# Performance work log

Hardware: AMD Instinct MI355X
Metric: run time of the kernel (lower is better)

## Reference

```python
import jax, jax.numpy as jnp
import numpy as np

EPSILON_BASE = 0.1
N_ITERS = 10


def setup_inputs() -> dict:
    key = jax.random.key(0)
    k1, k2 = jax.random.split(key)
    N, D = 8192, 512
    embeddings = jax.random.normal(k1, (N, D), dtype=jnp.float32)
    target_noise = jax.random.normal(k2, (N, D), dtype=jnp.float32)
    return {"embeddings": embeddings, "target_noise": target_noise}


def _l2_normalize(x, axis=1, eps=1e-12):
    # matches torch.nn.functional.normalize (divide by max(norm, eps))
    norm = jnp.sqrt(jnp.sum(x * x, axis=axis, keepdims=True))
    return x / jnp.maximum(norm, eps)


def _sinkhorn(x, y):
    n, d = x.shape
    # normalize_embeddings=True path
    x = _l2_normalize(x, axis=1)
    y = _l2_normalize(y, axis=1)
    epsilon = EPSILON_BASE * 2.0
    # squared euclidean cost: C[i,j] = ||x_i - y_j||^2  (cdist p=2, squared)
    sq_x = jnp.sum(x * x, axis=1, keepdims=True)          # (n,1)
    sq_y = jnp.sum(y * y, axis=1, keepdims=True)          # (n,1)
    C = jnp.maximum(sq_x + sq_y.T - 2.0 * (x @ y.T), 0.0)  # (n,n)
    log_K = -C / epsilon

    def body(carry, _):
        log_u, log_v = carry
        log_u = -jax.nn.logsumexp(log_K + log_v[None, :], axis=1)
        log_v = -jax.nn.logsumexp(log_K.T + log_u[None, :], axis=1)
        return (log_u, log_v), None

    init = (jnp.zeros(n, dtype=x.dtype), jnp.zeros(n, dtype=y.dtype))
    (log_u, log_v), _ = jax.lax.scan(body, init, None, length=N_ITERS)

    log_P = log_u[:, None] + log_K + log_v[None, :]
    P = jnp.clip(jnp.exp(log_P), 0.0, 1.0)
    distance = jnp.sum(P * C) / n

    # nan/inf fallback: 1 - mean cosine similarity (x, y already unit norm)
    fallback = 1.0 - jnp.mean(jnp.sum(x * y, axis=1))
    bad = jnp.isnan(distance) | jnp.isinf(distance)
    return jnp.where(bad, fallback, distance)


def reference(embeddings, target_noise):
    if embeddings.ndim == 3:
        embeddings = embeddings.reshape(-1, embeddings.shape[-1])
        target_noise = target_noise.reshape(-1, target_noise.shape[-1])
    return _sinkhorn(embeddings, target_noise)
```

## Files before the change

### kernel.cpp

```cpp
#include <hip/hip_runtime.h>
#include <hip/hip_bf16.h>
#include <stdint.h>

#define NROW 8192
#define DIM  512
#define LN2   0.6931471805599453f
#define TEN_LOG2E 14.426950408889634f

typedef __attribute__((ext_vector_type(8))) short short8;
typedef __attribute__((ext_vector_type(4))) float f32x4;
typedef __attribute__((ext_vector_type(2))) float f32x2;

__global__ __launch_bounds__(256) void init_kernel(float* __restrict__ v,
                                                   float* __restrict__ diagacc,
                                                   float* __restrict__ distacc) {
  const int g = blockIdx.x * 256 + threadIdx.x;
  v[g] = 1.0f;
  if (g == 0) { diagacc[0] = 0.f; distacc[0] = 0.f; }
}

__global__ __launch_bounds__(256) void normalize_kernel(
    const float* __restrict__ X, const float* __restrict__ Y,
    __hip_bfloat16* __restrict__ Xn, __hip_bfloat16* __restrict__ Yn,
    float* __restrict__ diagacc) {
  const int wave = threadIdx.x >> 6, lane = threadIdx.x & 63;
  float dsum = 0.f;
  #pragma unroll
  for (int rr = 0; rr < 4; rr++) {
    const int row = blockIdx.x * 16 + wave * 4 + rr;
    const float4* xr = (const float4*)(X + (size_t)row * DIM);
    const float4* yr = (const float4*)(Y + (size_t)row * DIM);
    float4 x0 = xr[lane], x1 = xr[lane + 64];
    float4 y0 = yr[lane], y1 = yr[lane + 64];
    float sx = x0.x*x0.x + x0.y*x0.y + x0.z*x0.z + x0.w*x0.w
             + x1.x*x1.x + x1.y*x1.y + x1.z*x1.z + x1.w*x1.w;
    float sy = y0.x*y0.x + y0.y*y0.y + y0.z*y0.z + y0.w*y0.w
             + y1.x*y1.x + y1.y*y1.y + y1.z*y1.z + y1.w*y1.w;
    float sxy = x0.x*y0.x + x0.y*y0.y + x0.z*y0.z + x0.w*y0.w
              + x1.x*y1.x + x1.y*y1.y + x1.z*y1.z + x1.w*y1.w;
    #pragma unroll
    for (int off = 1; off < 64; off <<= 1) {
      sx  += __shfl_xor(sx, off, 64);
      sy  += __shfl_xor(sy, off, 64);
      sxy += __shfl_xor(sxy, off, 64);
    }
    const float rx = 1.0f / fmaxf(sqrtf(sx), 1e-12f);
    const float ry = 1.0f / fmaxf(sqrtf(sy), 1e-12f);
    if (lane == 0) dsum += sxy * rx * ry;
    ushort4 px, py;
    { __hip_bfloat16 b;
      b = __float2bfloat16(x0.x*rx); px.x = *(unsigned short*)&b;
      b = __float2bfloat16(x0.y*rx); px.y = *(unsigned short*)&b;
      b = __float2bfloat16(x0.z*rx); px.z = *(unsigned short*)&b;
      b = __float2bfloat16(x0.w*rx); px.w = *(unsigned short*)&b;
      b = __float2bfloat16(y0.x*ry); py.x = *(unsigned short*)&b;
      b = __float2bfloat16(y0.y*ry); py.y = *(unsigned short*)&b;
      b = __float2bfloat16(y0.z*ry); py.z = *(unsigned short*)&b;
      b = __float2bfloat16(y0.w*ry); py.w = *(unsigned short*)&b;
    }
    ((ushort4*)(Xn + (size_t)row * DIM))[lane] = px;
    ((ushort4*)(Yn + (size_t)row * DIM))[lane] = py;
    { __hip_bfloat16 b;
      b = __float2bfloat16(x1.x*rx); px.x = *(unsigned short*)&b;
      b = __float2bfloat16(x1.y*rx); px.y = *(unsigned short*)&b;
      b = __float2bfloat16(x1.z*rx); px.z = *(unsigned short*)&b;
      b = __float2bfloat16(x1.w*rx); px.w = *(unsigned short*)&b;
      b = __float2bfloat16(y1.x*ry); py.x = *(unsigned short*)&b;
      b = __float2bfloat16(y1.y*ry); py.y = *(unsigned short*)&b;
      b = __float2bfloat16(y1.z*ry); py.z = *(unsigned short*)&b;
      b = __float2bfloat16(y1.w*ry); py.w = *(unsigned short*)&b;
    }
    ((ushort4*)(Xn + (size_t)row * DIM))[lane + 64] = px;
    ((ushort4*)(Yn + (size_t)row * DIM))[lane + 64] = py;
  }
  if (lane == 0) atomicAdd(diagacc, dsum);
}

__global__ __launch_bounds__(256) void gemm_kernel(
    const __hip_bfloat16* __restrict__ A, const __hip_bfloat16* __restrict__ B,
    uint8_t* __restrict__ K) {
  __shared__ __align__(16) char smem[20480];
  short* As = (short*)smem;
  short* Bs = (short*)(smem + 10240);
  int* tileT = (int*)smem;

  const int m0 = blockIdx.y * 128;
  const int n0 = blockIdx.x * 128;
  const int t = threadIdx.x;
  const int wave = t >> 6, lane = t & 63;
  const int wm = (wave & 1) * 64, wn = (wave >> 1) * 64;
  const int fr = lane & 15;
  const int fq = lane >> 4;

  f32x4 acc[4][4];
  #pragma unroll
  for (int i = 0; i < 4; i++)
    #pragma unroll
    for (int j = 0; j < 4; j++) acc[i][j] = (f32x4)0.f;

  const int L0 = t, L1 = t + 256;
  const int ar0 = L0 >> 2, ac0 = L0 & 3;
  const int ar1 = L1 >> 2, ac1 = L1 & 3;
  const int4* Ag = (const int4*)A;
  const int4* Bg = (const int4*)B;

  for (int kt = 0; kt < 16; ++kt) {
    const int kb = kt * 4;
    int4 a0 = Ag[(size_t)(m0 + ar0) * 64 + kb + ac0];
    int4 a1 = Ag[(size_t)(m0 + ar1) * 64 + kb + ac1];
    int4 b0 = Bg[(size_t)(n0 + ar0) * 64 + kb + ac0];
    int4 b1 = Bg[(size_t)(n0 + ar1) * 64 + kb + ac1];
    __syncthreads();
    ((int4*)As)[ar0 * 5 + ac0] = a0;
    ((int4*)As)[ar1 * 5 + ac1] = a1;
    ((int4*)Bs)[ar0 * 5 + ac0] = b0;
    ((int4*)Bs)[ar1 * 5 + ac1] = b1;
    __syncthreads();
    short8 af[4], bfr[4];
    #pragma unroll
    for (int i = 0; i < 4; i++) {
      af[i]  = *(const short8*)&As[(wm + i * 16 + fr) * 40 + fq * 8];
      bfr[i] = *(const short8*)&Bs[(wn + i * 16 + fr) * 40 + fq * 8];
    }
    #pragma unroll
    for (int i = 0; i < 4; i++)
      #pragma unroll
      for (int j = 0; j < 4; j++)
        acc[i][j] = __builtin_amdgcn_mfma_f32_16x16x32_bf16(af[i], bfr[j], acc[i][j], 0, 0, 0);
  }
  __syncthreads();
  #pragma unroll
  for (int i = 0; i < 4; i++) {
    #pragma unroll
    for (int j = 0; j < 4; j++) {
      const int Rq = (wm >> 2) + i * 4 + fq;
      const int Cc = wn + j * 16 + fr;
      float v0 = exp2f(fminf(acc[i][j][0], 1.0f) * TEN_LOG2E);
      float v1 = exp2f(fminf(acc[i][j][1], 1.0f) * TEN_LOG2E);
      float v2 = exp2f(fminf(acc[i][j][2], 1.0f) * TEN_LOG2E);
      float v3 = exp2f(fminf(acc[i][j][3], 1.0f) * TEN_LOG2E);
      int pk = 0;
      pk = __builtin_amdgcn_cvt_pk_fp8_f32(v0, v1, pk, false);
      pk = __builtin_amdgcn_cvt_pk_fp8_f32(v2, v3, pk, true);
      tileT[Cc * 33 + Rq] = pk;
    }
  }
  __syncthreads();
  const int rl = t >> 1;
  const int half = t & 1;
  const int rq = rl >> 2;
  const int rb = (rl & 3) * 8;
  uint8_t* Krow = K + (size_t)(m0 + rl) * NROW + n0 + half * 64;
  #pragma unroll
  for (int q = 0; q < 4; q++) {
    int out[4];
    #pragma unroll
    for (int d = 0; d < 4; d++) {
      const int c0 = (half * 16 + q * 4 + d) * 4;
      const unsigned w0 = (unsigned)tileT[(c0 + 0) * 33 + rq];
      const unsigned w1 = (unsigned)tileT[(c0 + 1) * 33 + rq];
      const unsigned w2 = (unsigned)tileT[(c0 + 2) * 33 + rq];
      const unsigned w3 = (unsigned)tileT[(c0 + 3) * 33 + rq];
      out[d] = (int)(((w0 >> rb) & 0xffu) | (((w1 >> rb) & 0xffu) << 8)
                   | (((w2 >> rb) & 0xffu) << 16) | (((w3 >> rb) & 0xffu) << 24));
    }
    int4 o; o.x = out[0]; o.y = out[1]; o.z = out[2]; o.w = out[3];
    ((int4*)Krow)[q] = o;
  }
}

__global__ __launch_bounds__(512) void fused_pass_kernel(
    const uint8_t* __restrict__ K, const float* __restrict__ v,
    float* __restrict__ u, float* __restrict__ partials) {
  __shared__ float wsum[8][8];
  __shared__ float ubc[8];
  const int t = threadIdx.x;
  const int wave = t >> 6, lane = t & 63;
  const int i0 = blockIdx.x * 32;

  float wv[16];
  {
    const float4* vp = (const float4*)(v + t * 16);
    ((float4*)wv)[0] = vp[0]; ((float4*)wv)[1] = vp[1];
    ((float4*)wv)[2] = vp[2]; ((float4*)wv)[3] = vp[3];
  }
  float acc[16];
  #pragma unroll
  for (int c = 0; c < 16; c++) acc[c] = 0.f;

  for (int b = 0; b < 4; b++) {
    const int rbase = i0 + b * 8;
    int4 kd[8];
    #pragma unroll
    for (int r = 0; r < 8; r++)
      kd[r] = *(const int4*)(K + (size_t)(rbase + r) * NROW + t * 16);
    float dot[8];
    #pragma unroll
    for (int r = 0; r < 8; r++) {
      const int* kp = (const int*)&kd[r];
      float d0 = 0.f, d1 = 0.f;
      #pragma unroll
      for (int q = 0; q < 4; q++) {
        f32x2 lo = __builtin_amdgcn_cvt_pk_f32_fp8(kp[q], false);
        f32x2 hi = __builtin_amdgcn_cvt_pk_f32_fp8(kp[q], true);
        d0 += lo.x * wv[4 * q] + lo.y * wv[4 * q + 1];
        d1 += hi.x * wv[4 * q + 2] + hi.y * wv[4 * q + 3];
      }
      dot[r] = d0 + d1;
    }
    #pragma unroll
    for (int r = 0; r < 8; r++)
      #pragma unroll
      for (int off = 1; off < 64; off <<= 1)
        dot[r] += __shfl_xor(dot[r], off, 64);
    if (lane == 0) {
      #pragma unroll
      for (int r = 0; r < 8; r++) wsum[wave][r] = dot[r];
    }
    __syncthreads();
    if (t < 8) {
      float s = wsum[0][t] + wsum[1][t] + wsum[2][t] + wsum[3][t]
              + wsum[4][t] + wsum[5][t] + wsum[6][t] + wsum[7][t];
      float uu = 1.0f / s;
      ubc[t] = uu;
      u[rbase + t] = uu;
    }
    __syncthreads();
    float ur[8];
    #pragma unroll
    for (int r = 0; r < 8; r++) ur[r] = ubc[r];
    #pragma unroll
    for (int r = 0; r < 8; r++) {
      const int* kp = (const int*)&kd[r];
      #pragma unroll
      for (int q = 0; q < 4; q++) {
        f32x2 lo = __builtin_amdgcn_cvt_pk_f32_fp8(kp[q], false);
        f32x2 hi = __builtin_amdgcn_cvt_pk_f32_fp8(kp[q], true);
        acc[4 * q]     += lo.x * ur[r];
        acc[4 * q + 1] += lo.y * ur[r];
        acc[4 * q + 2] += hi.x * ur[r];
        acc[4 * q + 3] += hi.y * ur[r];
      }
    }
  }
  float4* pp = (float4*)(partials + (size_t)blockIdx.x * NROW + t * 16);
  pp[0] = ((float4*)acc)[0]; pp[1] = ((float4*)acc)[1];
  pp[2] = ((float4*)acc)[2]; pp[3] = ((float4*)acc)[3];
}

__global__ __launch_bounds__(256) void vreduce_kernel(
    const float* __restrict__ partials, float* __restrict__ v) {
  const int j = blockIdx.x * 256 + threadIdx.x;
  float s = 0.f;
  #pragma unroll 8
  for (int p = 0; p < 256; p++) s += partials[(size_t)p * NROW + j];
  v[j] = 1.0f / s;
}

__global__ __launch_bounds__(512) void dist_kernel(
    const uint8_t* __restrict__ K, const float* __restrict__ v,
    const float* __restrict__ u, float* __restrict__ distacc) {
  __shared__ float uld[32];
  const int t = threadIdx.x;
  const int i0 = blockIdx.x * 32;
  if (t < 32) uld[t] = u[i0 + t];
  float wv[16];
  {
    const float4* vp = (const float4*)(v + t * 16);
    ((float4*)wv)[0] = vp[0]; ((float4*)wv)[1] = vp[1];
    ((float4*)wv)[2] = vp[2]; ((float4*)wv)[3] = vp[3];
  }
  __syncthreads();
  float acc = 0.f;
  #pragma unroll 4
  for (int r = 0; r < 32; r++) {
    int4 kd = *(const int4*)(K + (size_t)(i0 + r) * NROW + t * 16);
    const float ui = uld[r];
    const int* kp = (const int*)&kd;
    #pragma unroll
    for (int q = 0; q < 4; q++) {
      f32x2 lo = __builtin_amdgcn_cvt_pk_f32_fp8(kp[q], false);
      f32x2 hi = __builtin_amdgcn_cvt_pk_f32_fp8(kp[q], true);
      float kvv[4] = {lo.x, lo.y, hi.x, hi.y};
      #pragma unroll
      for (int e = 0; e < 4; e++) {
        float kk = kvv[e];
        float p = fminf(ui * kk * wv[4 * q + e], 1.f);
        float ct = 2.f - 0.2f * LN2 * __log2f(fmaxf(kk, 1e-6f));
        acc += p * ct;
      }
    }
  }
  #pragma unroll
  for (int off = 32; off > 0; off >>= 1) acc += __shfl_down(acc, off, 64);
  __shared__ float sb[8];
  const int wave = t >> 6;
  if ((t & 63) == 0) sb[wave] = acc;
  __syncthreads();
  if (t == 0) {
    float tot = sb[0] + sb[1] + sb[2] + sb[3] + sb[4] + sb[5] + sb[6] + sb[7];
    atomicAdd(distacc, tot);
  }
}

__global__ void final_kernel(const float* __restrict__ distacc,
                             const float* __restrict__ diagacc,
                             float* __restrict__ out) {
  if (threadIdx.x == 0 && blockIdx.x == 0) {
    float d = distacc[0] * (1.0f / (float)NROW);
    float fb = 1.0f - diagacc[0] * (1.0f / (float)NROW);
    float v = (isnan(d) || isinf(d)) ? fb : d;
    __hip_bfloat16 b = __float2bfloat16(v);
    unsigned short h = *(unsigned short*)&b;
    ((unsigned int*)out)[0] = ((unsigned int)h << 16) | (unsigned int)h;
  }
}

extern "C" void kernel_launch(void* const* d_in, const int* in_sizes, int n_in,
                              void* d_out, int out_size, void* d_ws, size_t ws_size,
                              hipStream_t stream) {
  (void)in_sizes; (void)n_in; (void)out_size; (void)ws_size;
  const float* X = (const float*)d_in[0];
  const float* Y = (const float*)d_in[1];
  float* out = (float*)d_out;

  char* ws = (char*)d_ws;
  size_t off = 0;
  uint8_t* K = (uint8_t*)(ws + off);                off += (size_t)NROW * NROW;
  float* partials = (float*)(ws + off);             off += (size_t)256 * NROW * 4;
  __hip_bfloat16* Xn = (__hip_bfloat16*)(ws + off); off += (size_t)NROW * DIM * 2;
  __hip_bfloat16* Yn = (__hip_bfloat16*)(ws + off); off += (size_t)NROW * DIM * 2;
  float* uvec = (float*)(ws + off); off += NROW * 4;
  float* vvec = (float*)(ws + off); off += NROW * 4;
  float* diagacc = (float*)(ws + off); off += 256;
  float* distacc = (float*)(ws + off); off += 256;

  init_kernel<<<32, 256, 0, stream>>>(vvec, diagacc, distacc);
  normalize_kernel<<<512, 256, 0, stream>>>(X, Y, Xn, Yn, diagacc);
  gemm_kernel<<<dim3(64, 64), 256, 0, stream>>>(Xn, Yn, K);
  for (int it = 0; it < 10; ++it) {
    fused_pass_kernel<<<256, 512, 0, stream>>>(K, vvec, uvec, partials);
    vreduce_kernel<<<32, 256, 0, stream>>>(partials, vvec);
  }
  dist_kernel<<<256, 512, 0, stream>>>(K, vvec, uvec, distacc);
  final_kernel<<<1, 64, 0, stream>>>(distacc, diagacc, out);
}
```

Before: 539.1 us.

## Halve rows per block in Sinkhorn passes, split vreduce, and fix GEMM epilogue transpose

The fused row/column pass and the distance kernel now process 16 rows per block instead of 32, which doubles the grid to 512 blocks so the GPU's CUs are better filled. Each pass writes twice as many partial column sums, so the partials buffer grows and vreduce now spreads its 512 partials over 8 thread groups, combining them in shared memory across 256 blocks instead of 32. Separately, the GEMM epilogue stores its fp8 tile row-major in shared memory and reads it back with vector loads in place of strided scalar reads. The trade-off is twice the partial-sum write and read traffic per iteration.

```diff
diff --git a/kernel.cpp b/kernel.cpp
--- a/kernel.cpp
+++ b/kernel.cpp
@@ -142,7 +142,7 @@
       int pk = 0;
       pk = __builtin_amdgcn_cvt_pk_fp8_f32(v0, v1, pk, false);
       pk = __builtin_amdgcn_cvt_pk_fp8_f32(v2, v3, pk, true);
-      tileT[Cc * 33 + Rq] = pk;
+      tileT[Rq * 132 + Cc] = pk;
     }
   }
   __syncthreads();
@@ -153,16 +153,20 @@
   uint8_t* Krow = K + (size_t)(m0 + rl) * NROW + n0 + half * 64;
   #pragma unroll
   for (int q = 0; q < 4; q++) {
+    const int base = rq * 132 + half * 64 + q * 16;
+    int4 w0 = *(const int4*)&tileT[base];
+    int4 w1 = *(const int4*)&tileT[base + 4];
+    int4 w2 = *(const int4*)&tileT[base + 8];
+    int4 w3 = *(const int4*)&tileT[base + 12];
     int out[4];
+    const int* wp[4] = {(const int*)&w0, (const int*)&w1, (const int*)&w2, (const int*)&w3};
     #pragma unroll
     for (int d = 0; d < 4; d++) {
-      const int c0 = (half * 16 + q * 4 + d) * 4;
-      const unsigned w0 = (unsigned)tileT[(c0 + 0) * 33 + rq];
-      const unsigned w1 = (unsigned)tileT[(c0 + 1) * 33 + rq];
-      const unsigned w2 = (unsigned)tileT[(c0 + 2) * 33 + rq];
-      const unsigned w3 = (unsigned)tileT[(c0 + 3) * 33 + rq];
-      out[d] = (int)(((w0 >> rb) & 0xffu) | (((w1 >> rb) & 0xffu) << 8)
-                   | (((w2 >> rb) & 0xffu) << 16) | (((w3 >> rb) & 0xffu) << 24));
+      const unsigned a0 = ((unsigned)wp[d][0] >> rb) & 0xffu;
+      const unsigned a1 = ((unsigned)wp[d][1] >> rb) & 0xffu;
+      const unsigned a2 = ((unsigned)wp[d][2] >> rb) & 0xffu;
+      const unsigned a3 = ((unsigned)wp[d][3] >> rb) & 0xffu;
+      out[d] = (int)(a0 | (a1 << 8) | (a2 << 16) | (a3 << 24));
     }
     int4 o; o.x = out[0]; o.y = out[1]; o.z = out[2]; o.w = out[3];
     ((int4*)Krow)[q] = o;
@@ -176,7 +180,7 @@
   __shared__ float ubc[8];
   const int t = threadIdx.x;
   const int wave = t >> 6, lane = t & 63;
-  const int i0 = blockIdx.x * 32;
+  const int i0 = blockIdx.x * 16;
 
   float wv[16];
   {
@@ -188,7 +192,8 @@
   #pragma unroll
   for (int c = 0; c < 16; c++) acc[c] = 0.f;
 
-  for (int b = 0; b < 4; b++) {
+  #pragma unroll
+  for (int b = 0; b < 2; b++) {
     const int rbase = i0 + b * 8;
     int4 kd[8];
     #pragma unroll
@@ -226,20 +231,18 @@
       u[rbase + t] = uu;
     }
     __syncthreads();
-    float ur[8];
-    #pragma unroll
-    for (int r = 0; r < 8; r++) ur[r] = ubc[r];
     #pragma unroll
     for (int r = 0; r < 8; r++) {
+      const float ur = ubc[r];
       const int* kp = (const int*)&kd[r];
       #pragma unroll
       for (int q = 0; q < 4; q++) {
         f32x2 lo = __builtin_amdgcn_cvt_pk_f32_fp8(kp[q], false);
         f32x2 hi = __builtin_amdgcn_cvt_pk_f32_fp8(kp[q], true);
-        acc[4 * q]     += lo.x * ur[r];
-        acc[4 * q + 1] += lo.y * ur[r];
-        acc[4 * q + 2] += hi.x * ur[r];
-        acc[4 * q + 3] += hi.y * ur[r];
+        acc[4 * q]     += lo.x * ur;
+        acc[4 * q + 1] += lo.y * ur;
+        acc[4 * q + 2] += hi.x * ur;
+        acc[4 * q + 3] += hi.y * ur;
       }
     }
   }
@@ -250,20 +253,30 @@
 
 __global__ __launch_bounds__(256) void vreduce_kernel(
     const float* __restrict__ partials, float* __restrict__ v) {
-  const int j = blockIdx.x * 256 + threadIdx.x;
+  __shared__ float red[8][32];
+  const int t = threadIdx.x;
+  const int c = t & 31, g = t >> 5;
+  const int j = blockIdx.x * 32 + c;
   float s = 0.f;
   #pragma unroll 8
-  for (int p = 0; p < 256; p++) s += partials[(size_t)p * NROW + j];
-  v[j] = 1.0f / s;
+  for (int p = g * 64; p < g * 64 + 64; p++) s += partials[(size_t)p * NROW + j];
+  red[g][c] = s;
+  __syncthreads();
+  if (t < 32) {
+    float tot = 0.f;
+    #pragma unroll
+    for (int gg = 0; gg < 8; gg++) tot += red[gg][t];
+    v[blockIdx.x * 32 + t] = 1.0f / tot;
+  }
 }
 
 __global__ __launch_bounds__(512) void dist_kernel(
     const uint8_t* __restrict__ K, const float* __restrict__ v,
     const float* __restrict__ u, float* __restrict__ distacc) {
-  __shared__ float uld[32];
+  __shared__ float uld[16];
   const int t = threadIdx.x;
-  const int i0 = blockIdx.x * 32;
-  if (t < 32) uld[t] = u[i0 + t];
+  const int i0 = blockIdx.x * 16;
+  if (t < 16) uld[t] = u[i0 + t];
   float wv[16];
   {
     const float4* vp = (const float4*)(v + t * 16);
@@ -273,7 +286,7 @@
   __syncthreads();
   float acc = 0.f;
   #pragma unroll 4
-  for (int r = 0; r < 32; r++) {
+  for (int r = 0; r < 16; r++) {
     int4 kd = *(const int4*)(K + (size_t)(i0 + r) * NROW + t * 16);
     const float ui = uld[r];
     const int* kp = (const int*)&kd;
@@ -327,7 +340,7 @@
   char* ws = (char*)d_ws;
   size_t off = 0;
   uint8_t* K = (uint8_t*)(ws + off);                off += (size_t)NROW * NROW;
-  float* partials = (float*)(ws + off);             off += (size_t)256 * NROW * 4;
+  float* partials = (float*)(ws + off);             off += (size_t)512 * NROW * 4;
   __hip_bfloat16* Xn = (__hip_bfloat16*)(ws + off); off += (size_t)NROW * DIM * 2;
   __hip_bfloat16* Yn = (__hip_bfloat16*)(ws + off); off += (size_t)NROW * DIM * 2;
   float* uvec = (float*)(ws + off); off += NROW * 4;
@@ -339,9 +352,9 @@
   normalize_kernel<<<512, 256, 0, stream>>>(X, Y, Xn, Yn, diagacc);
   gemm_kernel<<<dim3(64, 64), 256, 0, stream>>>(Xn, Yn, K);
   for (int it = 0; it < 10; ++it) {
-    fused_pass_kernel<<<256, 512, 0, stream>>>(K, vvec, uvec, partials);
-    vreduce_kernel<<<32, 256, 0, stream>>>(partials, vvec);
-  }
-  dist_kernel<<<256, 512, 0, stream>>>(K, vvec, uvec, distacc);
+    fused_pass_kernel<<<512, 512, 0, stream>>>(K, vvec, uvec, partials);
+    vreduce_kernel<<<256, 256, 0, stream>>>(partials, vvec);
+  }
+  dist_kernel<<<512, 512, 0, stream>>>(K, vvec, uvec, distacc);
   final_kernel<<<1, 64, 0, stream>>>(distacc, diagacc, out);
 }
```

Measured after the change: 720.8 us. +33.7%, slower.
